# Optimization experiments

Hardware: AMD Instinct MI355X
Metric: run time of the kernel (lower is better)

## Reference

```python
import jax, jax.numpy as jnp
import numpy as np

DIVIDE = 1.0


def setup_inputs() -> dict:
    key = jax.random.key(0)
    ks = jax.random.split(key, 12)
    B, NH, L, H, DIM = 2, 8, 1024, 64, 64
    return {
        "mask": jax.random.normal(ks[0], (B, NH, L, L), dtype=jnp.float32),
        "q": jax.random.normal(ks[1], (B, L, NH, H), dtype=jnp.float32),
        "k": jax.random.normal(ks[2], (B, L, NH, H), dtype=jnp.float32),
        "v": jax.random.normal(ks[3], (B, L, NH, H), dtype=jnp.float32),
        "W0": jax.random.normal(ks[4], (1, DIM), dtype=jnp.float32) * 0.02,
        "b0": jnp.zeros((DIM,), dtype=jnp.float32),
        "W1": jax.random.normal(ks[5], (DIM, DIM), dtype=jnp.float32) * 0.02,
        "b1": jnp.zeros((DIM,), dtype=jnp.float32),
        "W2": jax.random.normal(ks[6], (DIM, DIM), dtype=jnp.float32) * 0.02,
        "b2": jnp.zeros((DIM,), dtype=jnp.float32),
        "Wf": jax.random.normal(ks[7], (DIM, 8), dtype=jnp.float32) * 0.02,
        "bf": jnp.zeros((8,), dtype=jnp.float32),
    }


def reference(mask, q, k, v, W0, b0, W1, b1, W2, b2, Wf, bf):
    # default positions: arange over L1 / L2; identical across batch so we
    # compute the (L1, L2) relative-position grid once and broadcast.
    L1, L2 = q.shape[-3], k.shape[-3]
    pos_q = jnp.arange(L1, dtype=q.dtype)
    pos_k = jnp.arange(L2, dtype=q.dtype)
    rel = (pos_q[:, None] - pos_k[None, :]) / DIVIDE          # (L1, L2)
    rel = rel[..., None]                                       # (L1, L2, 1)
    # depth-3 MLP: Linear -> SiLU (norm=False => Identity), final Linear to n_heads
    h = jax.nn.silu(rel @ W0 + b0)                             # (L1, L2, DIM)
    h = jax.nn.silu(h @ W1 + b1)
    h = jax.nn.silu(h @ W2 + b2)
    bias = h @ Wf + bf                                         # (L1, L2, NH)
    bias = jnp.moveaxis(bias, -1, 0)                           # (NH, L1, L2)
    # mask shapes already match q/k lengths -> no padding branch needed
    return mask - bias                                          # broadcast over B
```

## Files before the change

kernel.cpp:

```cpp
#include <hip/hip_runtime.h>
#include <hip/hip_bf16.h>


#define L_SEQ 1024
#define NDIAG (2 * L_SEQ - 1)
#define NH 8
#define DIM 64

typedef float f32x4 __attribute__((ext_vector_type(4)));

__device__ __forceinline__ float silu_f(float x) {
    return x / (1.0f + __expf(-x));
}

__global__ __launch_bounds__(256) void build_bias_table(
    const float* __restrict__ W0, const float* __restrict__ b0,
    const float* __restrict__ W1, const float* __restrict__ b1,
    const float* __restrict__ W2, const float* __restrict__ b2,
    const float* __restrict__ Wf, const float* __restrict__ bf,
    float* __restrict__ tab ) {
    const int g = threadIdx.x >> 6;
    const int t = threadIdx.x & 63;
    const int d = blockIdx.x * 4 + g;
    const float rel = (float)(d - (L_SEQ - 1));

    __shared__ float sh[4][DIM];

    float h = silu_f(rel * W0[t] + b0[t]);
    sh[g][t] = h;
    __syncthreads();

    float acc = b1[t];
    #pragma unroll
    for (int k = 0; k < DIM; ++k) acc += sh[g][k] * W1[k * DIM + t];
    float h1 = silu_f(acc);
    __syncthreads();
    sh[g][t] = h1;
    __syncthreads();

    acc = b2[t];
    #pragma unroll
    for (int k = 0; k < DIM; ++k) acc += sh[g][k] * W2[k * DIM + t];
    float h2 = silu_f(acc);
    __syncthreads();
    sh[g][t] = h2;
    __syncthreads();

    if (t < NH && d < NDIAG) {
        float a = bf[t];
        #pragma unroll
        for (int k = 0; k < DIM; ++k) a += sh[g][k] * Wf[k * NH + t];
        tab[t * NDIAG + d] = a;
    }
}

__global__ __launch_bounds__(256) void apply_bias(
    const f32x4* __restrict__ mask, const float* __restrict__ tab,
    f32x4* __restrict__ out, int half4) {
    const int idx = blockIdx.x * 256 + threadIdx.x;

    #pragma unroll
    for (int p = 0; p < 2; ++p) {
        const int id = idx + p * half4;
        const int n = id << 2;
        const int j = n & (L_SEQ - 1);
        const int i = (n >> 10) & (L_SEQ - 1);
        const int h = (n >> 20) & (NH - 1);
        const float* tb = tab + h * NDIAG + (i - j + (L_SEQ - 1));
        const f32x4 m = __builtin_nontemporal_load(&mask[id]);
        f32x4 o;
        o.x = m.x - tb[0];
        o.y = m.y - tb[-1];
        o.z = m.z - tb[-2];
        o.w = m.w - tb[-3];
        __builtin_nontemporal_store(o, &out[id]);
    }
}

extern "C" void kernel_launch(void* const* d_in, const int* in_sizes, int n_in,
                              void* d_out, int out_size, void* d_ws, size_t ws_size,
                              hipStream_t stream) {
    const float* mask = (const float*)d_in[0];
    const float* W0 = (const float*)d_in[4];
    const float* b0 = (const float*)d_in[5];
    const float* W1 = (const float*)d_in[6];
    const float* b1 = (const float*)d_in[7];
    const float* W2 = (const float*)d_in[8];
    const float* b2 = (const float*)d_in[9];
    const float* Wf = (const float*)d_in[10];
    const float* bf = (const float*)d_in[11];
    float* out = (float*)d_out;

    float* tab = (float*)d_ws;

    build_bias_table<<<(NDIAG + 3) / 4, 256, 0, stream>>>(
        W0, b0, W1, b1, W2, b2, Wf, bf, tab);

    const int n4 = out_size / 4;
    const int half4 = n4 / 2;
    const int grid = half4 / 256;
    apply_bias<<<grid, 256, 0, stream>>>(
        (const f32x4*)mask, tab, (f32x4*)out, half4);
}
```

Baseline: 32.96 us.

## Store bias table reversed and map one block per row for ascending reads

The bias table is now written in reversed diagonal order, so each output row reads a contiguous, ascending window of it. The apply kernel assigns one block per (batch, head, row) and one f32x4 per thread, replacing the two-element-per-thread flattened indexing. Nontemporal loads and stores become ordinary loads and stores. The aim is simpler index math and coalesced forward table reads, at the cost of twice as many blocks and possible cache pollution from the streaming mask traffic.

```diff
diff --git a/kernel.cpp b/kernel.cpp
--- a/kernel.cpp
+++ b/kernel.cpp
@@ -18,7 +18,7 @@
     const float* __restrict__ W1, const float* __restrict__ b1,
     const float* __restrict__ W2, const float* __restrict__ b2,
     const float* __restrict__ Wf, const float* __restrict__ bf,
-    float* __restrict__ tab ) {
+    float* __restrict__ rtab ) {
     const int g = threadIdx.x >> 6;
     const int t = threadIdx.x & 63;
     const int d = blockIdx.x * 4 + g;
@@ -50,31 +50,29 @@
         float a = bf[t];
         #pragma unroll
         for (int k = 0; k < DIM; ++k) a += sh[g][k] * Wf[k * NH + t];
-        tab[t * NDIAG + d] = a;
+        rtab[t * NDIAG + (NDIAG - 1 - d)] = a;
     }
 }
 
 __global__ __launch_bounds__(256) void apply_bias(
-    const f32x4* __restrict__ mask, const float* __restrict__ tab,
-    f32x4* __restrict__ out, int half4) {
-    const int idx = blockIdx.x * 256 + threadIdx.x;
+    const f32x4* __restrict__ mask, const float* __restrict__ rtab,
+    f32x4* __restrict__ out) {
+    const int row = blockIdx.x;
+    const int i = row & (L_SEQ - 1);
+    const int h = (row >> 10) & (NH - 1);
+    const float* rt = rtab + h * NDIAG + (L_SEQ - 1 - i);
 
-    #pragma unroll
-    for (int p = 0; p < 2; ++p) {
-        const int id = idx + p * half4;
-        const int n = id << 2;
-        const int j = n & (L_SEQ - 1);
-        const int i = (n >> 10) & (L_SEQ - 1);
-        const int h = (n >> 20) & (NH - 1);
-        const float* tb = tab + h * NDIAG + (i - j + (L_SEQ - 1));
-        const f32x4 m = __builtin_nontemporal_load(&mask[id]);
-        f32x4 o;
-        o.x = m.x - tb[0];
-        o.y = m.y - tb[-1];
-        o.z = m.z - tb[-2];
-        o.w = m.w - tb[-3];
-        __builtin_nontemporal_store(o, &out[id]);
-    }
+    const int t = threadIdx.x;
+    const int idx = row * 256 + t;
+    const int j0 = t << 2;
+
+    const f32x4 m = mask[idx];
+    f32x4 o;
+    o.x = m.x - rt[j0 + 0];
+    o.y = m.y - rt[j0 + 1];
+    o.z = m.z - rt[j0 + 2];
+    o.w = m.w - rt[j0 + 3];
+    out[idx] = o;
 }
 
 extern "C" void kernel_launch(void* const* d_in, const int* in_sizes, int n_in,
@@ -91,14 +89,12 @@
     const float* bf = (const float*)d_in[11];
     float* out = (float*)d_out;
 
-    float* tab = (float*)d_ws;
+    float* rtab = (float*)d_ws;
 
     build_bias_table<<<(NDIAG + 3) / 4, 256, 0, stream>>>(
-        W0, b0, W1, b1, W2, b2, Wf, bf, tab);
+        W0, b0, W1, b1, W2, b2, Wf, bf, rtab);
 
-    const int n4 = out_size / 4;
-    const int half4 = n4 / 2;
-    const int grid = half4 / 256;
-    apply_bias<<<grid, 256, 0, stream>>>(
-        (const f32x4*)mask, tab, (f32x4*)out, half4);
+    const int rows = out_size / L_SEQ;
+    apply_bias<<<rows, 256, 0, stream>>>(
+        (const f32x4*)mask, rtab, (f32x4*)out);
 }
```

New measurement: 31.26 us. 5.2% less time.
